# Kernel optimization log

Hardware: AMD Instinct MI355X
Metric: run time of the kernel (lower is better)

The kernel has to match this reference:

```python
import jax, jax.numpy as jnp
import numpy as np

# ---- static config (matches init_kwargs) ----
B, S, D = 2, 4096, 1024          # batch, seq_len, dim_input
L, ST = 512, 64                  # segment_len, state_len
H = 8                            # num_heads
DK0, DV0, DK1, DV1 = 64, 64, 64, 64  # per-head key/value dims for 2 memory levels
DH = 4096                        # dim_hidden (MLP)
T = 2 * ST + L                   # tokens per segment block: [state, segment, state]


def setup_inputs() -> dict:
    key = jax.random.key(0)
    ks = jax.random.split(key, 18)
    f32 = jnp.float32
    def w(k, shape, fan_in):
        return (jax.random.normal(k, shape, dtype=f32) / np.float32(np.sqrt(fan_in)))
    return {
        "x": jax.random.normal(ks[0], (B, S, D), dtype=f32),
        "state_init": 0.02 * jax.random.normal(ks[1], (ST, D), dtype=f32),
        # level-0 projections: dim_input -> per-head (key/value)
        "Wq0": w(ks[2], (D, H, DK0), D),
        "Wk0": w(ks[3], (D, H, DK0), D),
        "Wv0": w(ks[4], (D, H, DV0), D),
        # level-1 projections: level-0 value dim -> per-head (key/value)
        "Wq1": w(ks[5], (H, DV0, DK1), DV0),
        "Wk1": w(ks[6], (H, DV0, DK1), DV0),
        "Wv1": w(ks[7], (H, DV0, DV1), DV0),
        # output projection back to dim_input
        "Wo": w(ks[8], (H, DV1, D), H * DV1),
        "bo": jnp.zeros((D,), f32),
        "g_attn": jnp.ones((D,), f32),
        "b_attn": jnp.zeros((D,), f32),
        "W1": w(ks[9], (D, DH), D),
        "b1": jnp.zeros((DH,), f32),
        "W2": w(ks[10], (DH, D), DH),
        "b2": jnp.zeros((D,), f32),
        "g_mlp": jnp.ones((D,), f32),
        "b_mlp": jnp.zeros((D,), f32),
    }


def _layernorm(x, g, b, eps=1e-5):
    mu = jnp.mean(x, axis=-1, keepdims=True)
    var = jnp.mean(jnp.square(x - mu), axis=-1, keepdims=True)
    return (x - mu) * jax.lax.rsqrt(var + eps) * g + b


def _rope(x, pos):
    # x: (B, H, T, dk); rotary embedding with base 10000
    dk = x.shape[-1]
    inv_freq = jnp.power(jnp.float32(10000.0), -jnp.arange(0, dk, 2, dtype=jnp.float32) / dk)
    ang = pos[:, None] * inv_freq[None, :]              # (T, dk/2)
    cos, sin = jnp.cos(ang), jnp.sin(ang)
    x1, x2 = x[..., 0::2], x[..., 1::2]
    r1 = x1 * cos - x2 * sin
    r2 = x1 * sin + x2 * cos
    return jnp.stack([r1, r2], axis=-1).reshape(x.shape)


def _attend(q, k, v, mask):
    # q,k: (B,H,T,dk); v: (B,H,T,dv); causal mask (T,T)
    scale = jnp.float32(1.0 / np.sqrt(q.shape[-1]))
    scores = jnp.einsum('bhqc,bhkc->bhqk', q, k) * scale
    scores = jnp.where(mask, scores, jnp.float32(-1e30))
    p = jax.nn.softmax(scores, axis=-1)
    return jnp.einsum('bhqk,bhkv->bhqv', p, v)


def _remmtas(x, state_init, Wq0, Wk0, Wv0, Wq1, Wk1, Wv1, Wo, bo):
    b, s, d = x.shape
    n_seg = s // L
    xs = x.reshape(b, n_seg, L, d).transpose(1, 0, 2, 3)   # (n_seg, B, L, D)
    mask = jnp.tril(jnp.ones((T, T), dtype=bool))
    pos = jnp.arange(T, dtype=jnp.float32)
    state0 = jnp.broadcast_to(state_init, (b, ST, d))

    def step(state, seg):
        toks = jnp.concatenate([state, seg, state], axis=1)      # (B, T, D)
        # memory level 0
        q0 = _rope(jnp.einsum('btd,dhk->bhtk', toks, Wq0), pos)
        k0 = _rope(jnp.einsum('btd,dhk->bhtk', toks, Wk0), pos)
        v0 = jnp.einsum('btd,dhv->bhtv', toks, Wv0)
        o0 = _attend(q0, k0, v0, mask)                           # (B,H,T,DV0)
        # memory level 1 (consumes level-0 values, per-head)
        q1 = _rope(jnp.einsum('bhtv,hvk->bhtk', o0, Wq1), pos)
        k1 = _rope(jnp.einsum('bhtv,hvk->bhtk', o0, Wk1), pos)
        v1 = jnp.einsum('bhtv,hvw->bhtw', o0, Wv1)
        o1 = _attend(q1, k1, v1, mask)                           # (B,H,T,DV1)
        out = jnp.einsum('bhtv,hvd->btd', o1, Wo) + bo           # (B,T,D)
        new_state = out[:, ST + L:]                              # trailing state tokens
        return new_state, out[:, ST:ST + L]                      # segment output

    _, outs = jax.lax.scan(step, state0, xs)                     # (n_seg, B, L, D)
    return outs.transpose(1, 0, 2, 3).reshape(b, s, d)


def reference(x, state_init, Wq0, Wk0, Wv0, Wq1, Wk1, Wv1, Wo, bo,
              g_attn, b_attn, W1, b1, W2, b2, g_mlp, b_mlp):
    a = _remmtas(x, state_init, Wq0, Wk0, Wv0, Wq1, Wk1, Wv1, Wo, bo)
    h = _layernorm(a + x, g_attn, b_attn)
    m = jax.nn.gelu(h @ W1 + b1, approximate=False) @ W2 + b2
    # note: second residual adds the ORIGINAL x, per the source code
    return _layernorm(m + x, g_mlp, b_mlp)
```

## Files before the change

### kernel.cpp

```cpp
#include <hip/hip_runtime.h>
#include <hip/hip_bf16.h>

typedef __hip_bfloat16 bf16;
typedef short bf16x8 __attribute__((ext_vector_type(8)));
typedef float f32x4 __attribute__((ext_vector_type(4)));

#define CB 2
#define CS 4096
#define CD 1024
#define CL 512
#define CST 64
#define CH 8
#define CT 640
#define CDH 4096
#define NSEG 8
#define LP 80

__device__ __forceinline__ float tof(float x) { return x; }
__device__ __forceinline__ float tof(bf16 x) { return __bfloat162float(x); }
__device__ __forceinline__ void storev(float* p, float v) { *p = v; }
__device__ __forceinline__ void storev(bf16* p, float v) { *p = __float2bfloat16(v); }

__device__ __forceinline__ float ldin(const void* p, size_t i, int f32w) {
    if (f32w) return ((const float*)p)[i];
    return __bfloat162float(((const bf16*)p)[i]);
}

__global__ void sniff_kernel(const void* x, int* flag) {
    if (threadIdx.x == 0 && blockIdx.x == 0) {
        const bf16* hb = (const bf16*)x;
        int plaus = 0;
        for (int i = 0; i < 256; ++i) {
            float v = __bfloat162float(hb[2 * i]);
            float a = fabsf(v);
            if (v == 0.f || (a > 1e-4f && a < 100.f)) ++plaus;
        }
        flag[0] = (plaus < 128) ? 1 : 0;
    }
}

__global__ __launch_bounds__(256) void transpose_kernel(
    const void* __restrict__ in, bf16* __restrict__ out, int R, int C,
    const int* __restrict__ flag)
{
    const int f32w = flag[0];
    __shared__ short t[64][72];
    int tid = threadIdx.x;
    int c0 = blockIdx.x * 64, r0 = blockIdx.y * 64;
    int cc = tid & 63, rr = tid >> 6;
#pragma unroll
    for (int i = 0; i < 16; ++i) {
        bf16 v = __float2bfloat16(ldin(in, (size_t)(r0 + rr + i * 4) * C + c0 + cc, f32w));
        t[rr + i * 4][cc] = *(short*)&v;
    }
    __syncthreads();
#pragma unroll
    for (int i = 0; i < 16; ++i)
        ((short*)out)[(size_t)(c0 + rr + i * 4) * R + r0 + cc] = t[cc][rr + i * 4];
}

__global__ __launch_bounds__(256) void transpose3_kernel(
    const void* __restrict__ in0, const void* __restrict__ in1, const void* __restrict__ in2,
    bf16* __restrict__ out0, bf16* __restrict__ out1, bf16* __restrict__ out2,
    const int* __restrict__ flag)
{
    const int f32w = flag[0];
    const void* in = (blockIdx.z == 0) ? in0 : (blockIdx.z == 1 ? in1 : in2);
    bf16* out = (blockIdx.z == 0) ? out0 : (blockIdx.z == 1 ? out1 : out2);
    const int R = CD, C = 512;
    __shared__ short t[64][72];
    int tid = threadIdx.x;
    int c0 = blockIdx.x * 64, r0 = blockIdx.y * 64;
    int cc = tid & 63, rr = tid >> 6;
#pragma unroll
    for (int i = 0; i < 16; ++i) {
        bf16 v = __float2bfloat16(ldin(in, (size_t)(r0 + rr + i * 4) * C + c0 + cc, f32w));
        t[rr + i * 4][cc] = *(short*)&v;
    }
    __syncthreads();
#pragma unroll
    for (int i = 0; i < 16; ++i)
        ((short*)out)[(size_t)(c0 + rr + i * 4) * R + r0 + cc] = t[cc][rr + i * 4];
}

__global__ __launch_bounds__(256) void transposeH_kernel(
    const void* __restrict__ Wq1, const void* __restrict__ Wk1, const void* __restrict__ Wv1,
    bf16* __restrict__ oq, bf16* __restrict__ ok, bf16* __restrict__ ov,
    const int* __restrict__ flag)
{
    const int f32w = flag[0];
    int which = blockIdx.x >> 3, hh = blockIdx.x & 7;
    const void* in = (which == 0) ? Wq1 : (which == 1) ? Wk1 : Wv1;
    bf16* out = (which == 0) ? oq : (which == 1) ? ok : ov;
    __shared__ short t[64][72];
    int tid = threadIdx.x;
    int cc = tid & 63, rr = tid >> 6;
    size_t base = (size_t)hh * 4096;
#pragma unroll
    for (int i = 0; i < 16; ++i) {
        bf16 v = __float2bfloat16(ldin(in, base + (size_t)(rr + i * 4) * 64 + cc, f32w));
        t[rr + i * 4][cc] = *(short*)&v;
    }
    __syncthreads();
#pragma unroll
    for (int i = 0; i < 16; ++i)
        ((short*)out)[base + (size_t)(rr + i * 4) * 64 + cc] = t[cc][rr + i * 4];
}

template <typename TC, int ACT, int OUTM, int ACCUM>
__global__ __launch_bounds__(256) void mfma_lds(
    const bf16* __restrict__ A,
    const bf16* __restrict__ Bt0, const bf16* __restrict__ Bt1, const bf16* __restrict__ Bt2,
    TC* __restrict__ C0, TC* __restrict__ C1, TC* __restrict__ C2,
    float* __restrict__ ST,
    const void* __restrict__ bias, int boff,
    int M, int N, int K, int lda, int ldb, int seg,
    const int* __restrict__ flag)
{
    const int f32w = flag[0];
    const bf16* Bt = (blockIdx.z == 0) ? Bt0 : (blockIdx.z == 1 ? Bt1 : Bt2);
    TC* C = (blockIdx.z == 0) ? C0 : (blockIdx.z == 1 ? C1 : C2);

    __shared__ __align__(16) short As[128 * 64];
    __shared__ __align__(16) short Bs[128 * 64];

    const int tid = threadIdx.x;
    const int lane = tid & 63;
    const int w = tid >> 6;
    const int wm = w >> 1, wn = w & 1;
    const int bm = blockIdx.x * 128, bn = blockIdx.y * 128;

    f32x4 acc[4][4];
#pragma unroll
    for (int i = 0; i < 4; ++i)
#pragma unroll
        for (int j = 0; j < 4; ++j) acc[i][j] = (f32x4){0.f, 0.f, 0.f, 0.f};

    int srow[4], skc[4];
#pragma unroll
    for (int i = 0; i < 4; ++i) {
        int c = i * 256 + tid;
        srow[i] = c >> 3;
        skc[i] = (c & 7) * 8;
    }

    bf16x8 rA0[4], rB0[4], rA1[4], rB1[4];
#pragma unroll
    for (int i = 0; i < 4; ++i) {
        rA0[i] = *(const bf16x8*)(A + (size_t)(bm + srow[i]) * lda + skc[i]);
        rB0[i] = *(const bf16x8*)(Bt + (size_t)(bn + srow[i]) * ldb + skc[i]);
        rA1[i] = *(const bf16x8*)(A + (size_t)(bm + srow[i]) * lda + 64 + skc[i]);
        rB1[i] = *(const bf16x8*)(Bt + (size_t)(bn + srow[i]) * ldb + 64 + skc[i]);
    }

#define MFMA_PHASE                                                              \
    _Pragma("unroll")                                                           \
    for (int kh = 0; kh < 2; ++kh) {                                            \
        bf16x8 av[4], bv[4];                                                    \
        _Pragma("unroll")                                                       \
        for (int mi = 0; mi < 4; ++mi) {                                        \
            int r = wm * 64 + mi * 16 + (lane & 15);                            \
            int cl = kh * 4 + (lane >> 4);                                      \
            av[mi] = *(const bf16x8*)&As[r * 64 + cl * 8];                      \
        }                                                                       \
        _Pragma("unroll")                                                       \
        for (int nj = 0; nj < 4; ++nj) {                                        \
            int r = wn * 64 + nj * 16 + (lane & 15);                            \
            int cl = kh * 4 + (lane >> 4);                                      \
            bv[nj] = *(const bf16x8*)&Bs[r * 64 + cl * 8];                      \
        }                                                                       \
        _Pragma("unroll")                                                       \
        for (int mi = 0; mi < 4; ++mi)                                          \
            _Pragma("unroll")                                                   \
            for (int nj = 0; nj < 4; ++nj)                                      \
                acc[mi][nj] = __builtin_amdgcn_mfma_f32_16x16x32_bf16(          \
                    av[mi], bv[nj], acc[mi][nj], 0, 0, 0);                      \
    }

    for (int k0 = 0; k0 < K; k0 += 128) {
        __syncthreads();
#pragma unroll
        for (int i = 0; i < 4; ++i) {
            *(bf16x8*)&As[(size_t)(i * 256 + tid) * 8] = rA0[i];
            *(bf16x8*)&Bs[(size_t)(i * 256 + tid) * 8] = rB0[i];
        }
        if (k0 + 128 < K) {
            int kn = k0 + 128;
#pragma unroll
            for (int i = 0; i < 4; ++i) {
                rA0[i] = *(const bf16x8*)(A + (size_t)(bm + srow[i]) * lda + kn + skc[i]);
                rB0[i] = *(const bf16x8*)(Bt + (size_t)(bn + srow[i]) * ldb + kn + skc[i]);
            }
        }
        __syncthreads();
        MFMA_PHASE

        __syncthreads();
#pragma unroll
        for (int i = 0; i < 4; ++i) {
            *(bf16x8*)&As[(size_t)(i * 256 + tid) * 8] = rA1[i];
            *(bf16x8*)&Bs[(size_t)(i * 256 + tid) * 8] = rB1[i];
        }
        if (k0 + 192 < K) {
            int kn = k0 + 192;
#pragma unroll
            for (int i = 0; i < 4; ++i) {
                rA1[i] = *(const bf16x8*)(A + (size_t)(bm + srow[i]) * lda + kn + skc[i]);
                rB1[i] = *(const bf16x8*)(Bt + (size_t)(bn + srow[i]) * ldb + kn + skc[i]);
            }
        }
        __syncthreads();
        MFMA_PHASE
    }
#undef MFMA_PHASE

#pragma unroll
    for (int mi = 0; mi < 4; ++mi) {
#pragma unroll
        for (int nj = 0; nj < 4; ++nj) {
            int c = bn + wn * 64 + nj * 16 + (lane & 15);
            float bia = bias ? ldin(bias, boff + c, f32w) : 0.f;
#pragma unroll
            for (int r = 0; r < 4; ++r) {
                int row = bm + wm * 64 + mi * 16 + (lane >> 4) * 4 + r;
                float v = acc[mi][nj][r] + bia;
                if (ACT == 1) v = 0.5f * v * (1.0f + erff(v * 0.70710678118654752f));
                if (OUTM == 0) {
                    if (ACCUM) v += tof(C[(size_t)row * N + c]);
                    storev(C + (size_t)row * N + c, v);
                } else {
                    ST[(size_t)row * CD + c] = v;
                }
            }
        }
    }
}

__global__ __launch_bounds__(256) void ropeV_kernel(
    bf16* __restrict__ q, bf16* __restrict__ k,
    const bf16* __restrict__ v, bf16* __restrict__ vt)
{
    int t0 = blockIdx.x * 64, hh = blockIdx.y, b = blockIdx.z;
    int tid = threadIdx.x;
    __shared__ short lt[64][72];
    int c = tid & 63;
    int r0 = tid >> 6;
    int ip = c >> 1;
    float inv = powf(10000.f, -(float)(2 * ip) / 64.f);
#pragma unroll
    for (int i = 0; i < 16; ++i) {
        int r = r0 + i * 4;
        int t = t0 + r;
        size_t idx = ((size_t)b * CT + t) * 512 + hh * 64 + c;
        float qv = tof(q[idx]);
        float kv = tof(k[idx]);
        float ang = (float)t * inv;
        float sn, cs;
        sincosf(ang, &sn, &cs);
        float qp = __shfl_xor(qv, 1);
        float kp = __shfl_xor(kv, 1);
        float rq, rk;
        if (c & 1) { rq = qp * sn + qv * cs; rk = kp * sn + kv * cs; }
        else       { rq = qv * cs - qp * sn; rk = kv * cs - kp * sn; }
        q[idx] = __float2bfloat16(rq);
        k[idx] = __float2bfloat16(rk);
        lt[r][c] = ((const short*)v)[idx];
    }
    __syncthreads();
#pragma unroll
    for (int i = 0; i < 16; ++i) {
        int c2 = r0 + i * 4;
        int r2 = c;
        ((short*)vt)[((size_t)(b * CH + hh) * 64 + c2) * CT + t0 + r2] = lt[r2][c2];
    }
}

template <int FUSE>
__global__ __launch_bounds__(256) void attn_mfma(
    const bf16* __restrict__ q, const bf16* __restrict__ k, const bf16* __restrict__ vt,
    bf16* __restrict__ o,
    int qsb, int qsh, int qst,
    int ksb, int ksh, int kst,
    int seg,
    const bf16* __restrict__ Wq1t, const bf16* __restrict__ Wk1t, const bf16* __restrict__ Wv1t,
    bf16* __restrict__ q1o, bf16* __restrict__ k1o, bf16* __restrict__ v1to)
{
    const int tid = threadIdx.x;
    const int lane = tid & 63;
    const int wrow = tid >> 6;
    const int hh = blockIdx.y, b = blockIdx.z;
    const int qbase = (FUSE ? ((int)gridDim.x - 1 - (int)blockIdx.x)
                            : ((int)gridDim.x - (int)blockIdx.x)) * 64;

    __shared__ __align__(16) short Qs[64 * LP];
    __shared__ __align__(16) short Ks[64 * LP];
    __shared__ __align__(16) short Vs[64 * LP];
    __shared__ __align__(16) short Ps[64 * LP];

    const size_t qb0 = (size_t)b * qsb + (size_t)hh * qsh;
    const size_t kb0 = (size_t)b * ksb + (size_t)hh * ksh;
    const size_t vtb = (size_t)(b * CH + hh) * 64 * CT;

    int srow[2], skc[2], soff[2];
#pragma unroll
    for (int i = 0; i < 2; ++i) {
        int c = i * 256 + tid;
        srow[i] = c >> 3;
        skc[i] = c & 7;
        soff[i] = srow[i] * LP + skc[i] * 8;
    }

    bf16x8 rQ[2], rK[2], rV[2];
#pragma unroll
    for (int i = 0; i < 2; ++i) {
        rQ[i] = *(const bf16x8*)(q + qb0 + (size_t)(qbase + srow[i]) * qst + skc[i] * 8);
        rK[i] = *(const bf16x8*)(k + kb0 + (size_t)srow[i] * kst + skc[i] * 8);
        rV[i] = *(const bf16x8*)(vt + vtb + (size_t)srow[i] * CT + skc[i] * 8);
    }

    float mrow[4], lrow[4];
    f32x4 oacc[4];
#pragma unroll
    for (int r = 0; r < 4; ++r) { mrow[r] = -1e30f; lrow[r] = 0.f; }
#pragma unroll
    for (int nd = 0; nd < 4; ++nd) oacc[nd] = (f32x4){0.f, 0.f, 0.f, 0.f};

    const int ntiles = qbase / 64 + 1;
    for (int ti = 0; ti < ntiles; ++ti) {
        __syncthreads();
        if (ti == 0) {
#pragma unroll
            for (int i = 0; i < 2; ++i) *(bf16x8*)&Qs[soff[i]] = rQ[i];
        }
#pragma unroll
        for (int i = 0; i < 2; ++i) {
            *(bf16x8*)&Ks[soff[i]] = rK[i];
            *(bf16x8*)&Vs[soff[i]] = rV[i];
        }
        if (ti + 1 < ntiles) {
            int j1 = (ti + 1) * 64;
#pragma unroll
            for (int i = 0; i < 2; ++i) {
                rK[i] = *(const bf16x8*)(k + kb0 + (size_t)(j1 + srow[i]) * kst + skc[i] * 8);
                rV[i] = *(const bf16x8*)(vt + vtb + (size_t)srow[i] * CT + j1 + skc[i] * 8);
            }
        }
        __syncthreads();

        f32x4 sacc[4];
#pragma unroll
        for (int nj = 0; nj < 4; ++nj) sacc[nj] = (f32x4){0.f, 0.f, 0.f, 0.f};
#pragma unroll
        for (int kh = 0; kh < 2; ++kh) {
            int cl = kh * 4 + (lane >> 4);
            bf16x8 av = *(const bf16x8*)&Qs[(wrow * 16 + (lane & 15)) * LP + cl * 8];
#pragma unroll
            for (int nj = 0; nj < 4; ++nj) {
                bf16x8 bv = *(const bf16x8*)&Ks[(nj * 16 + (lane & 15)) * LP + cl * 8];
                sacc[nj] = __builtin_amdgcn_mfma_f32_16x16x32_bf16(av, bv, sacc[nj], 0, 0, 0);
            }
        }

        const bool diag = (ti == ntiles - 1);
        float pm[4] = {-1e30f, -1e30f, -1e30f, -1e30f};
#pragma unroll
        for (int nj = 0; nj < 4; ++nj) {
            int col_l = nj * 16 + (lane & 15);
#pragma unroll
            for (int r = 0; r < 4; ++r) {
                int row_l = wrow * 16 + ((lane >> 4) << 2) + r;
                float s = (diag && col_l > row_l) ? -1e30f : sacc[nj][r] * 0.125f;
                sacc[nj][r] = s;
                pm[r] = fmaxf(pm[r], s);
            }
        }
#pragma unroll
        for (int msk = 1; msk < 16; msk <<= 1)
#pragma unroll
            for (int r = 0; r < 4; ++r) pm[r] = fmaxf(pm[r], __shfl_xor(pm[r], msk));

        float corr[4], rs[4] = {0.f, 0.f, 0.f, 0.f};
#pragma unroll
        for (int r = 0; r < 4; ++r) {
            float mn = fmaxf(mrow[r], pm[r]);
            corr[r] = __expf(mrow[r] - mn);
            mrow[r] = mn;
        }
#pragma unroll
        for (int nj = 0; nj < 4; ++nj)
#pragma unroll
            for (int r = 0; r < 4; ++r) {
                float p = __expf(sacc[nj][r] - mrow[r]);
                sacc[nj][r] = p;
                rs[r] += p;
            }
#pragma unroll
        for (int msk = 1; msk < 16; msk <<= 1)
#pragma unroll
            for (int r = 0; r < 4; ++r) rs[r] += __shfl_xor(rs[r], msk);
#pragma unroll
        for (int r = 0; r < 4; ++r) lrow[r] = lrow[r] * corr[r] + rs[r];
#pragma unroll
        for (int nd = 0; nd < 4; ++nd)
#pragma unroll
            for (int r = 0; r < 4; ++r) oacc[nd][r] *= corr[r];

#pragma unroll
        for (int nj = 0; nj < 4; ++nj)
#pragma unroll
            for (int r = 0; r < 4; ++r) {
                bf16 pb = __float2bfloat16(sacc[nj][r]);
                Ps[(wrow * 16 + ((lane >> 4) << 2) + r) * LP + nj * 16 + (lane & 15)] =
                    *(short*)&pb;
            }

#pragma unroll
        for (int kh = 0; kh < 2; ++kh) {
            int cl = kh * 4 + (lane >> 4);
            bf16x8 pa = *(const bf16x8*)&Ps[(wrow * 16 + (lane & 15)) * LP + cl * 8];
#pragma unroll
            for (int nd = 0; nd < 4; ++nd) {
                bf16x8 bv = *(const bf16x8*)&Vs[(nd * 16 + (lane & 15)) * LP + cl * 8];
                oacc[nd] = __builtin_amdgcn_mfma_f32_16x16x32_bf16(pa, bv, oacc[nd], 0, 0, 0);
            }
        }
    }

    if (FUSE == 0) {
        bf16* dst;
        int rbase;
        if (qbase == 576) { dst = q1o; rbase = b * 64 - 576; }
        else              { dst = o;   rbase = (b * 8 + seg) * 512 - 64; }
#pragma unroll
        for (int nd = 0; nd < 4; ++nd) {
#pragma unroll
            for (int r = 0; r < 4; ++r) {
                int row_g = qbase + wrow * 16 + ((lane >> 4) << 2) + r;
                int col = nd * 16 + (lane & 15);
                dst[(size_t)(rbase + row_g) * 512 + hh * 64 + col] =
                    __float2bfloat16(oacc[nd][r] / lrow[r]);
            }
        }
    } else {
#pragma unroll
        for (int nd = 0; nd < 4; ++nd)
#pragma unroll
            for (int r = 0; r < 4; ++r) {
                int row_l = wrow * 16 + ((lane >> 4) << 2) + r;
                bf16 ob16 = __float2bfloat16(oacc[nd][r] / lrow[r]);
                Qs[row_l * LP + nd * 16 + (lane & 15)] = *(short*)&ob16;
            }
        __syncthreads();

        const size_t whb = (size_t)hh * 4096;
        f32x4 qa[4], ka[4], va[4];
#pragma unroll
        for (int nj = 0; nj < 4; ++nj) {
            qa[nj] = (f32x4){0.f, 0.f, 0.f, 0.f};
            ka[nj] = (f32x4){0.f, 0.f, 0.f, 0.f};
            va[nj] = (f32x4){0.f, 0.f, 0.f, 0.f};
        }
#pragma unroll
        for (int kh = 0; kh < 2; ++kh) {
            int cl = kh * 4 + (lane >> 4);
            bf16x8 av = *(const bf16x8*)&Qs[(wrow * 16 + (lane & 15)) * LP + cl * 8];
#pragma unroll
            for (int nj = 0; nj < 4; ++nj) {
                int rowb = nj * 16 + (lane & 15);
                bf16x8 bq = *(const bf16x8*)(Wq1t + whb + (size_t)rowb * 64 + cl * 8);
                bf16x8 bk = *(const bf16x8*)(Wk1t + whb + (size_t)rowb * 64 + cl * 8);
                bf16x8 bw = *(const bf16x8*)(Wv1t + whb + (size_t)rowb * 64 + cl * 8);
                qa[nj] = __builtin_amdgcn_mfma_f32_16x16x32_bf16(av, bq, qa[nj], 0, 0, 0);
                ka[nj] = __builtin_amdgcn_mfma_f32_16x16x32_bf16(av, bk, ka[nj], 0, 0, 0);
                va[nj] = __builtin_amdgcn_mfma_f32_16x16x32_bf16(av, bw, va[nj], 0, 0, 0);
            }
        }
        const size_t bh = (size_t)(b * CH + hh);
#pragma unroll
        for (int nj = 0; nj < 4; ++nj) {
            int col = nj * 16 + (lane & 15);
            int ip = col >> 1;
            float inv = powf(10000.f, -(float)(2 * ip) / 64.f);
#pragma unroll
            for (int r = 0; r < 4; ++r) {
                int row_l = wrow * 16 + ((lane >> 4) << 2) + r;
                int t = qbase + row_l;
                float ang = (float)t * inv;
                float sn, cs;
                sincosf(ang, &sn, &cs);
                float aq = qa[nj][r], ak = ka[nj][r];
                float pq = __shfl_xor(aq, 1);
                float pk = __shfl_xor(ak, 1);
                float rq, rk;
                if (col & 1) { rq = pq * sn + aq * cs; rk = pk * sn + ak * cs; }
                else         { rq = aq * cs - pq * sn; rk = ak * cs - pk * sn; }
                size_t roff = (bh * CT + t) * 64 + col;
                q1o[roff] = __float2bfloat16(rq);
                k1o[roff] = __float2bfloat16(rk);
                v1to[(bh * 64 + col) * CT + t] = __float2bfloat16(va[nj][r]);
            }
        }
    }
}

__global__ __launch_bounds__(256) void build_toks_kernel(
    const void* __restrict__ x, const float* __restrict__ state, bf16* __restrict__ toks,
    int seg, const int* __restrict__ flag)
{
    const int f32w = flag[0];
    int idx = blockIdx.x * 256 + threadIdx.x;
    int d = idx & (CD - 1);
    int t = (idx >> 10) % CT;
    int b = idx / (CT * CD);
    float v;
    if (t < CST) v = state[(b * CST + t) * CD + d];
    else if (t < CST + CL) v = ldin(x, ((size_t)b * CS + seg * CL + (t - CST)) * CD + d, f32w);
    else v = state[(b * CST + (t - CST - CL)) * CD + d];
    toks[idx] = __float2bfloat16(v);
}

__global__ __launch_bounds__(256) void init_state_kernel(
    const void* __restrict__ s0, float* __restrict__ state, const int* __restrict__ flag)
{
    const int f32w = flag[0];
    int idx = blockIdx.x * 256 + threadIdx.x;
    state[idx] = ldin(s0, idx % (CST * CD), f32w);
}

__global__ __launch_bounds__(256) void ln_kernel(
    const bf16* __restrict__ ra, const void* __restrict__ x,
    const void* __restrict__ g, const void* __restrict__ bb,
    void* __restrict__ outp, int out_ext, const int* __restrict__ flag)
{
    const int f32w = flag[0];
    int row = blockIdx.x;
    int tid = threadIdx.x;
    __shared__ float buf[CD];
    __shared__ float red[4];

    float s = 0.f;
    for (int c = tid; c < CD; c += 256) {
        float v = tof(ra[(size_t)row * CD + c]) + ldin(x, (size_t)row * CD + c, f32w);
        buf[c] = v;
        s += v;
    }
#pragma unroll
    for (int off = 32; off; off >>= 1) s += __shfl_xor(s, off);
    if ((tid & 63) == 0) red[tid >> 6] = s;
    __syncthreads();
    float mu = (red[0] + red[1] + red[2] + red[3]) * (1.f / CD);
    __syncthreads();

    float vs = 0.f;
    for (int c = tid; c < CD; c += 256) {
        float d0 = buf[c] - mu;
        vs += d0 * d0;
    }
#pragma unroll
    for (int off = 32; off; off >>= 1) vs += __shfl_xor(vs, off);
    if ((tid & 63) == 0) red[tid >> 6] = vs;
    __syncthreads();
    float var = (red[0] + red[1] + red[2] + red[3]) * (1.f / CD);
    float rs = rsqrtf(var + 1e-5f);

    for (int c = tid; c < CD; c += 256) {
        float y = (buf[c] - mu) * rs * ldin(g, c, f32w) + ldin(bb, c, f32w);
        size_t idx = (size_t)row * CD + c;
        if (!out_ext) {
            ((bf16*)outp)[idx] = __float2bfloat16(y);
        } else if (f32w) {
            ((float*)outp)[idx] = y;
        } else {
            ((bf16*)outp)[idx] = __float2bfloat16(y);
        }
    }
}

extern "C" void kernel_launch(void* const* d_in, const int* in_sizes, int n_in,
                              void* d_out, int out_size, void* d_ws, size_t ws_size,
                              hipStream_t stream)
{
    const void* x      = d_in[0];
    const void* s0     = d_in[1];
    const void* Wq0    = d_in[2];
    const void* Wk0    = d_in[3];
    const void* Wv0    = d_in[4];
    const void* Wq1    = d_in[5];
    const void* Wk1    = d_in[6];
    const void* Wv1    = d_in[7];
    const void* Wo     = d_in[8];
    const void* bo     = d_in[9];
    const void* g_attn = d_in[10];
    const void* b_attn = d_in[11];
    const void* W1     = d_in[12];
    const void* b1     = d_in[13];
    const void* W2     = d_in[14];
    const void* b2     = d_in[15];
    const void* g_mlp  = d_in[16];
    const void* b_mlp  = d_in[17];

    int* flag = (int*)d_ws;
    float* f = (float*)((char*)d_ws + 16);
    float* toks_slot = f; f += (size_t)CB * CT * CD;
    float* q0_slot = f;  f += (size_t)CB * CH * CT * 64;
    float* k0_slot = f;  f += (size_t)CB * CH * CT * 64;
    float* v0_slot = f;  f += (size_t)CB * CH * CT * 64;
    float* o0_slot = f;  f += (size_t)CB * CH * CT * 64;
    float* q1_slot = f;  f += (size_t)CB * CH * CT * 64;
    float* k1_slot = f;  f += (size_t)CB * CH * CT * 64;
    float* v1_slot = f;  f += (size_t)CB * CH * CT * 64;
    float* o1t_slot = f; f += (size_t)CB * CT * (CH * 64);
    float* seg_slot = f; f += (size_t)CB * CT * CD;
    float* state = f;   f += (size_t)CB * CST * CD;
    float* a_slot = f;  f += (size_t)CB * CS * CD;
    bf16* h = (bf16*)f;
    bf16* tail = h + (size_t)CB * CS * CD;

    bf16* toks = (bf16*)toks_slot;
    bf16* q0b = (bf16*)q0_slot;
    bf16* k0b = (bf16*)k0_slot;
    bf16* v0b = (bf16*)v0_slot;
    bf16* v0t = (bf16*)o0_slot;
    bf16* q1b = (bf16*)q1_slot;
    bf16* k1b = (bf16*)k1_slot;
    bf16* v1t = (bf16*)v1_slot;
    bf16* ab  = (bf16*)a_slot;
    bf16* WtQ = h;
    bf16* WtK = WtQ + (size_t)512 * 1024;
    bf16* WtV = WtK + (size_t)512 * 1024;
    bf16* WtO = WtV + (size_t)512 * 1024;
    bf16* WtQ1 = WtO + (size_t)1024 * 512;
    bf16* WtK1 = WtQ1 + (size_t)8 * 4096;
    bf16* WtV1 = WtK1 + (size_t)8 * 4096;
    bf16* o1mid = WtV1 + (size_t)8 * 4096;
    bf16* o1s = o1mid + (size_t)CB * NSEG * 512 * 512;
    bf16* g1  = (bf16*)toks_slot;
    bf16* Wt1 = g1 + (size_t)CB * CS * CD;
    bf16* Wt2 = tail;

    sniff_kernel<<<1, 64, 0, stream>>>(x, flag);
    init_state_kernel<<<(CB * CST * CD) / 256, 256, 0, stream>>>(s0, state, flag);

    transpose3_kernel<<<dim3(8, 16, 3), 256, 0, stream>>>(
        Wq0, Wk0, Wv0, WtQ, WtK, WtV, flag);
    transpose_kernel<<<dim3(16, 8), 256, 0, stream>>>(Wo, WtO, 512, CD, flag);
    transposeH_kernel<<<24, 256, 0, stream>>>(Wq1, Wk1, Wv1, WtQ1, WtK1, WtV1, flag);
    transpose_kernel<<<dim3(CD / 64, CDH / 64), 256, 0, stream>>>(W2, Wt2, CDH, CD, flag);

    for (int seg = 0; seg < NSEG; ++seg) {
        build_toks_kernel<<<(CB * CT * CD) / 256, 256, 0, stream>>>(x, state, toks, seg, flag);
        mfma_lds<bf16, 0, 0, 0><<<dim3(10, 4, 3), 256, 0, stream>>>(
            toks, WtQ, WtK, WtV, q0b, k0b, v0b, nullptr, nullptr, 0,
            CB * CT, 512, CD, CD, CD, 0, flag);
        ropeV_kernel<<<dim3(CT / 64, CH, CB), 256, 0, stream>>>(q0b, k0b, v0b, v0t);
        attn_mfma<1><<<dim3(CT / 64, CH, CB), 256, 0, stream>>>(
            q0b, k0b, v0t, nullptr,
            CT * 512, 64, 512,
            CT * 512, 64, 512,
            seg,
            WtQ1, WtK1, WtV1, q1b, k1b, v1t);
        attn_mfma<0><<<dim3(9, CH, CB), 256, 0, stream>>>(
            q1b, k1b, v1t, o1mid,
            CH * CT * 64, CT * 64, 64,
            CH * CT * 64, CT * 64, 64,
            seg,
            nullptr, nullptr, nullptr, o1s, nullptr, nullptr);
        mfma_lds<bf16, 0, 2, 0><<<dim3(1, 8, 1), 256, 0, stream>>>(
            o1s, WtO, WtO, WtO, ab, ab, ab, state, bo, 0,
            128, CD, 512, 512, 512, seg, flag);
    }

    mfma_lds<bf16, 0, 0, 0><<<dim3(64, 8, 1), 256, 0, stream>>>(
        o1mid, WtO, WtO, WtO, ab, ab, ab, nullptr, bo, 0,
        CB * CS, CD, 512, 512, 512, 0, flag);

    ln_kernel<<<CB * CS, 256, 0, stream>>>(ab, x, g_attn, b_attn, h, 0, flag);

    transpose_kernel<<<dim3(CDH / 64, CD / 64), 256, 0, stream>>>(W1, Wt1, CD, CDH, flag);

    for (int c = 0; c < 4; ++c) {
        mfma_lds<bf16, 1, 0, 0><<<dim3(64, 8, 1), 256, 0, stream>>>(
            h, Wt1 + (size_t)c * 1024 * CD, Wt1, Wt1, g1, g1, g1, nullptr,
            b1, c * 1024, CB * CS, 1024, CD, CD, CD, 0, flag);
        if (c == 0)
            mfma_lds<bf16, 0, 0, 0><<<dim3(64, 8, 1), 256, 0, stream>>>(
                g1, Wt2 + (size_t)c * 1024, Wt2, Wt2, ab, ab, ab, nullptr,
                b2, 0, CB * CS, CD, 1024, 1024, CDH, 0, flag);
        else
            mfma_lds<bf16, 0, 0, 1><<<dim3(64, 8, 1), 256, 0, stream>>>(
                g1, Wt2 + (size_t)c * 1024, Wt2, Wt2, ab, ab, ab, nullptr,
                nullptr, 0, CB * CS, CD, 1024, 1024, CDH, 0, flag);
    }
    ln_kernel<<<CB * CS, 256, 0, stream>>>(ab, x, g_mlp, b_mlp, d_out, 1, flag);
}
```

Baseline: 1.150 ms.

## Load GEMM tiles directly into double-buffered, XOR-swizzled LDS via global_load_lds

The bf16 MFMA GEMM no longer stages tiles through registers. It uses the global_load_lds builtin to copy each 16-byte chunk straight from global memory into LDS, with two LDS buffers of 64-wide K tiles so the next tile's load is issued while the current one is being computed. LDS columns are XOR-swizzled by row to reduce bank conflicts on the MFMA operand reads, and each K step now needs one barrier instead of two. This cuts register pressure and VGPR-to-LDS store traffic, at the cost of twice the LDS use. It also relies on the compiler inserting the right wait counts so the asynchronous LDS writes are visible to other waves after the barrier.

```diff
diff --git a/kernel.cpp b/kernel.cpp
--- a/kernel.cpp
+++ b/kernel.cpp
@@ -26,6 +26,12 @@
     return __bfloat162float(((const bf16*)p)[i]);
 }
 
+__device__ __forceinline__ void gload16(const void* g, void* l) {
+    __builtin_amdgcn_global_load_lds(
+        (const __attribute__((address_space(1))) unsigned int*)g,
+        (__attribute__((address_space(3))) unsigned int*)l, 16, 0, 0);
+}
+
 __global__ void sniff_kernel(const void* x, int* flag) {
     if (threadIdx.x == 0 && blockIdx.x == 0) {
         const bf16* hb = (const bf16*)x;
@@ -121,14 +127,15 @@
     const bf16* Bt = (blockIdx.z == 0) ? Bt0 : (blockIdx.z == 1 ? Bt1 : Bt2);
     TC* C = (blockIdx.z == 0) ? C0 : (blockIdx.z == 1 ? C1 : C2);
 
-    __shared__ __align__(16) short As[128 * 64];
-    __shared__ __align__(16) short Bs[128 * 64];
+    __shared__ __align__(16) short As[2][128 * 64];
+    __shared__ __align__(16) short Bs[2][128 * 64];
 
     const int tid = threadIdx.x;
     const int lane = tid & 63;
     const int w = tid >> 6;
     const int wm = w >> 1, wn = w & 1;
     const int bm = blockIdx.x * 128, bn = blockIdx.y * 128;
+    const int ldsb = w * 2048;
 
     f32x4 acc[4][4];
 #pragma unroll
@@ -136,83 +143,55 @@
 #pragma unroll
         for (int j = 0; j < 4; ++j) acc[i][j] = (f32x4){0.f, 0.f, 0.f, 0.f};
 
-    int srow[4], skc[4];
+    int lr[4], lcq[4];
 #pragma unroll
     for (int i = 0; i < 4; ++i) {
-        int c = i * 256 + tid;
-        srow[i] = c >> 3;
-        skc[i] = (c & 7) * 8;
-    }
-
-    bf16x8 rA0[4], rB0[4], rA1[4], rB1[4];
+        int r = w * 32 + i * 8 + (lane >> 3);
+        lr[i] = r;
+        lcq[i] = ((lane & 7) ^ (r & 7)) * 8;
+    }
+
+    const int nt = K >> 6;
 #pragma unroll
     for (int i = 0; i < 4; ++i) {
-        rA0[i] = *(const bf16x8*)(A + (size_t)(bm + srow[i]) * lda + skc[i]);
-        rB0[i] = *(const bf16x8*)(Bt + (size_t)(bn + srow[i]) * ldb + skc[i]);
-        rA1[i] = *(const bf16x8*)(A + (size_t)(bm + srow[i]) * lda + 64 + skc[i]);
-        rB1[i] = *(const bf16x8*)(Bt + (size_t)(bn + srow[i]) * ldb + 64 + skc[i]);
-    }
-
-#define MFMA_PHASE                                                              \
-    _Pragma("unroll")                                                           \
-    for (int kh = 0; kh < 2; ++kh) {                                            \
-        bf16x8 av[4], bv[4];                                                    \
-        _Pragma("unroll")                                                       \
-        for (int mi = 0; mi < 4; ++mi) {                                        \
-            int r = wm * 64 + mi * 16 + (lane & 15);                            \
-            int cl = kh * 4 + (lane >> 4);                                      \
-            av[mi] = *(const bf16x8*)&As[r * 64 + cl * 8];                      \
-        }                                                                       \
-        _Pragma("unroll")                                                       \
-        for (int nj = 0; nj < 4; ++nj) {                                        \
-            int r = wn * 64 + nj * 16 + (lane & 15);                            \
-            int cl = kh * 4 + (lane >> 4);                                      \
-            bv[nj] = *(const bf16x8*)&Bs[r * 64 + cl * 8];                      \
-        }                                                                       \
-        _Pragma("unroll")                                                       \
-        for (int mi = 0; mi < 4; ++mi)                                          \
-            _Pragma("unroll")                                                   \
-            for (int nj = 0; nj < 4; ++nj)                                      \
-                acc[mi][nj] = __builtin_amdgcn_mfma_f32_16x16x32_bf16(          \
-                    av[mi], bv[nj], acc[mi][nj], 0, 0, 0);                      \
-    }
-
-    for (int k0 = 0; k0 < K; k0 += 128) {
+        gload16(A + (size_t)(bm + lr[i]) * lda + lcq[i], &As[0][ldsb + i * 512]);
+        gload16(Bt + (size_t)(bn + lr[i]) * ldb + lcq[i], &Bs[0][ldsb + i * 512]);
+    }
+
+    for (int t = 0; t < nt; ++t) {
         __syncthreads();
-#pragma unroll
-        for (int i = 0; i < 4; ++i) {
-            *(bf16x8*)&As[(size_t)(i * 256 + tid) * 8] = rA0[i];
-            *(bf16x8*)&Bs[(size_t)(i * 256 + tid) * 8] = rB0[i];
-        }
-        if (k0 + 128 < K) {
-            int kn = k0 + 128;
+        if (t + 1 < nt) {
+            const int kn = (t + 1) << 6;
+            const int nb = (t + 1) & 1;
 #pragma unroll
             for (int i = 0; i < 4; ++i) {
-                rA0[i] = *(const bf16x8*)(A + (size_t)(bm + srow[i]) * lda + kn + skc[i]);
-                rB0[i] = *(const bf16x8*)(Bt + (size_t)(bn + srow[i]) * ldb + kn + skc[i]);
-            }
-        }
-        __syncthreads();
-        MFMA_PHASE
-
-        __syncthreads();
-#pragma unroll
-        for (int i = 0; i < 4; ++i) {
-            *(bf16x8*)&As[(size_t)(i * 256 + tid) * 8] = rA1[i];
-            *(bf16x8*)&Bs[(size_t)(i * 256 + tid) * 8] = rB1[i];
-        }
-        if (k0 + 192 < K) {
-            int kn = k0 + 192;
-#pragma unroll
-            for (int i = 0; i < 4; ++i) {
-                rA1[i] = *(const bf16x8*)(A + (size_t)(bm + srow[i]) * lda + kn + skc[i]);
-                rB1[i] = *(const bf16x8*)(Bt + (size_t)(bn + srow[i]) * ldb + kn + skc[i]);
-            }
-        }
-        __syncthreads();
-        MFMA_PHASE
-    }
-#undef MFMA_PHASE
+                gload16(A + (size_t)(bm + lr[i]) * lda + kn + lcq[i], &As[nb][ldsb + i * 512]);
+                gload16(Bt + (size_t)(bn + lr[i]) * ldb + kn + lcq[i], &Bs[nb][ldsb + i * 512]);
+            }
+        }
+        const int cb = t & 1;
+#pragma unroll
+        for (int kh = 0; kh < 2; ++kh) {
+            bf16x8 av[4], bv[4];
+            const int cl = kh * 4 + (lane >> 4);
+#pragma unroll
+            for (int mi = 0; mi < 4; ++mi) {
+                int r = wm * 64 + mi * 16 + (lane & 15);
+                av[mi] = *(const bf16x8*)&As[cb][r * 64 + ((cl ^ (r & 7)) << 3)];
+            }
+#pragma unroll
+            for (int nj = 0; nj < 4; ++nj) {
+                int r = wn * 64 + nj * 16 + (lane & 15);
+                bv[nj] = *(const bf16x8*)&Bs[cb][r * 64 + ((cl ^ (r & 7)) << 3)];
+            }
+#pragma unroll
+            for (int mi = 0; mi < 4; ++mi)
+#pragma unroll
+                for (int nj = 0; nj < 4; ++nj)
+                    acc[mi][nj] = __builtin_amdgcn_mfma_f32_16x16x32_bf16(
+                        av[mi], bv[nj], acc[mi][nj], 0, 0, 0);
+        }
+    }
 
 #pragma unroll
     for (int mi = 0; mi < 4; ++mi) {
```

After: 1.136 ms. No clear change (-1.1%).
